# Kernel optimization log

Hardware: AMD Instinct MI355X
Metric: run time of the kernel (lower is better)

Reference implementation:

```python
import jax, jax.numpy as jnp
import numpy as np

B, K, D, H, R, MAXP, IMG = 8, 1024, 256, 8, 4, 1024, 224


def _ln(x, g, b, eps=1e-5):
    m = x.mean(-1, keepdims=True)
    v = ((x - m) ** 2).mean(-1, keepdims=True)
    return (x - m) / jnp.sqrt(v + eps) * g + b


def _rope2d(x, coords, cache, image_size):
    b, k, d = x.shape
    half, quarter = d // 2, d // 4
    maxp = cache.shape[0]
    cn = jnp.clip(coords.astype(jnp.float32) / image_size * (maxp - 1), 0, maxp - 1)
    y_idx = cn[..., 0].astype(jnp.int32)
    x_idx = cn[..., 1].astype(jnp.int32)
    yr = cache[y_idx]  # [B,K,quarter,2]
    xr = cache[x_idx]
    xp = x[..., :half].reshape(b, k, quarter, 2)
    yp = x[..., half:].reshape(b, k, quarter, 2)

    def rot(p, r):
        c, s = r[..., 0], r[..., 1]
        p0, p1 = p[..., 0], p[..., 1]
        return jnp.stack([p0 * c - p1 * s, p0 * s + p1 * c], -1).reshape(b, k, half)

    return jnp.concatenate([rot(xp, xr), rot(yp, yr)], -1)


def _mha_zero(xn, Wqkv, bqkv, Wo, bo, key_allowed, num_heads):
    # torch MultiheadAttention with an all-zero token appended to key/value
    # BEFORE projection -> extra key = b_k, extra value = b_v per head.
    b, l, d = xn.shape
    hd = d // num_heads
    Wq, Wk, Wv = jnp.split(Wqkv, 3, axis=0)
    bq, bk, bv = jnp.split(bqkv, 3)
    q = (xn @ Wq.T + bq).reshape(b, l, num_heads, hd)
    k = jnp.concatenate([xn @ Wk.T + bk, jnp.broadcast_to(bk, (b, 1, d))], 1)
    v = jnp.concatenate([xn @ Wv.T + bv, jnp.broadcast_to(bv, (b, 1, d))], 1)
    k = k.reshape(b, l + 1, num_heads, hd)
    v = v.reshape(b, l + 1, num_heads, hd)
    scores = jnp.einsum('bqhd,bkhd->bhqk', q, k) / jnp.sqrt(jnp.float32(hd))
    mask = jnp.concatenate([key_allowed, jnp.ones((b, 1), bool)], 1)  # zero slot always visible
    scores = jnp.where(mask[:, None, None, :], scores, -jnp.inf)
    attn = jax.nn.softmax(scores, axis=-1)
    out = jnp.einsum('bhqk,bkhd->bqhd', attn, v).reshape(b, l, d)
    return out @ Wo.T + bo


def setup_inputs() -> dict:
    key = jax.random.key(0)
    ks = jax.random.split(key, 20)
    x = jax.random.normal(ks[0], (B, K, D), dtype=jnp.float32)
    coords = jax.random.randint(ks[1], (B, K, 2), 0, IMG, dtype=jnp.int32)
    ctx_id_labels = jax.random.randint(ks[2], (B, K), 0, 2, dtype=jnp.int32)
    half = D // 2
    theta = 1.0 / (10000.0 ** (jnp.arange(0, half, 2, dtype=jnp.float32) / half))
    pos = jnp.arange(MAXP, dtype=jnp.float32)
    freqs = pos[:, None] * theta[None, :]
    rope_cache = jnp.stack([jnp.cos(freqs), jnp.sin(freqs)], -1)  # [MAXP, D/4, 2]
    s = 0.02
    return {
        'x': x, 'coords': coords, 'ctx_id_labels': ctx_id_labels,
        'target_embed': s * jax.random.normal(ks[3], (1, 1, D)),
        'context_embed': s * jax.random.normal(ks[4], (1, 1, D)),
        'register_tokens': s * jax.random.normal(ks[5], (1, R, D)),
        'rope_cache': rope_cache,
        'norm_g': jnp.ones((D,)), 'norm_b': jnp.zeros((D,)),
        'ctx_Wqkv': s * jax.random.normal(ks[6], (3 * D, D)),
        'ctx_bqkv': jnp.zeros((3 * D,)),
        'ctx_Wo': s * jax.random.normal(ks[7], (D, D)),
        'ctx_bo': jnp.zeros((D,)),
        'tgt_Wqkv': s * jax.random.normal(ks[8], (3 * D, D)),
        'tgt_bqkv': jnp.zeros((3 * D,)),
        'tgt_Wo': s * jax.random.normal(ks[9], (D, D)),
        'tgt_bo': jnp.zeros((D,)),
        'mlpn_g': jnp.ones((D,)), 'mlpn_b': jnp.zeros((D,)),
        'mlp_W1': s * jax.random.normal(ks[10], (4 * D, D)),
        'mlp_b1': jnp.zeros((4 * D,)),
        'mlp_W2': s * jax.random.normal(ks[11], (D, 4 * D)),
        'mlp_b2': jnp.zeros((D,)),
    }


def reference(x, coords, ctx_id_labels, target_embed, context_embed, register_tokens,
              rope_cache, norm_g, norm_b, ctx_Wqkv, ctx_bqkv, ctx_Wo, ctx_bo,
              tgt_Wqkv, tgt_bqkv, tgt_Wo, tgt_bo, mlpn_g, mlpn_b,
              mlp_W1, mlp_b1, mlp_W2, mlp_b2):
    b, k, d = x.shape
    is_ctx = ctx_id_labels > 0
    x = x + jnp.where(is_ctx[..., None], context_embed, target_embed)
    x = _rope2d(x, coords, rope_cache, IMG)
    registers = register_tokens + context_embed  # [1,R,D]
    x = jnp.concatenate([jnp.broadcast_to(registers, (b, R, d)), x], 1)
    is_ctx_f = jnp.concatenate([jnp.ones((b, R), bool), is_ctx], 1)
    xn = _ln(x, norm_g, norm_b)
    # ctx queries self-attend to context(+zero); tgt queries cross-attend to context(+zero)
    out_ctx = _mha_zero(xn, ctx_Wqkv, ctx_bqkv, ctx_Wo, ctx_bo, is_ctx_f, H)
    out_tgt = _mha_zero(xn, tgt_Wqkv, tgt_bqkv, tgt_Wo, tgt_bo, is_ctx_f, H)
    attn_out = jnp.where(is_ctx_f[..., None], out_ctx, out_tgt)
    attn_out = attn_out[:, R:]
    x = x[:, R:]
    x = x + attn_out
    h = _ln(x, mlpn_g, mlpn_b)
    h = jax.nn.gelu(h @ mlp_W1.T + mlp_b1, approximate=False) @ mlp_W2.T + mlp_b2
    return x + h
```

## Files before the change

### kernel.cpp

```cpp
#include <hip/hip_runtime.h>
#include <stdint.h>
#include <stddef.h>

typedef unsigned short u16;
typedef __bf16 bf16t;
typedef bf16t bf16x8 __attribute__((ext_vector_type(8)));
typedef u16 u16x8 __attribute__((ext_vector_type(8)));
typedef u16 u16x4 __attribute__((ext_vector_type(4)));
typedef float f32x4 __attribute__((ext_vector_type(4)));

__device__ __forceinline__ float bf2f(u16 u) {
  unsigned int x = ((unsigned int)u) << 16;
  return __builtin_bit_cast(float, x);
}
__device__ __forceinline__ u16 f2bf(float f) {
  unsigned int x = __builtin_bit_cast(unsigned int, f);
  x += 0x7fffu + ((x >> 16) & 1u);
  return (u16)(x >> 16);
}
__device__ __forceinline__ u16x8 ld8(const u16* p) { return *(const u16x8*)p; }

__device__ __forceinline__ f32x4 mfma_bf16(u16x8 a, u16x8 b, f32x4 c) {
  return __builtin_amdgcn_mfma_f32_16x16x32_bf16(
      __builtin_bit_cast(bf16x8, a), __builtin_bit_cast(bf16x8, b), c, 0, 0, 0);
}
__device__ __forceinline__ void g2lds16(const u16* g, u16* l) {
  __builtin_amdgcn_global_load_lds(
      (const __attribute__((address_space(1))) unsigned int*)g,
      (__attribute__((address_space(3))) unsigned int*)l, 16, 0, 0);
}
__device__ __forceinline__ void stc(u16* p, float v) { *p = f2bf(v); }
__device__ __forceinline__ void stc(float* p, float v) { *p = v; }

__device__ __forceinline__ float fast_erf(float x) {
  const float ax = fabsf(x);
  const float t = 1.0f / (1.0f + 0.3275911f * ax);
  const float y = 1.0f - (((((1.061405429f * t - 1.453152027f) * t) + 1.421413741f) * t
                  - 0.284496736f) * t + 0.254829592f) * t * __expf(-ax * ax);
  return copysignf(y, x);
}


__global__ __launch_bounds__(256) void cvt_kernel(
    const float* __restrict__ cW, const float* __restrict__ tW,
    const float* __restrict__ cWo_, const float* __restrict__ tWo_,
    const float* __restrict__ W1_, const float* __restrict__ W2_,
    const float* __restrict__ cb, const float* __restrict__ tb,
    u16* __restrict__ wA, u16* __restrict__ wB, u16* __restrict__ woc,
    u16* __restrict__ wot, u16* __restrict__ w1b, u16* __restrict__ w2b,
    float* __restrict__ bA, float* __restrict__ bB)
{
  const int blk = blockIdx.x;
  if (blk >= 1024) {
    const int e = threadIdx.x * 4;
    if (blk == 1024) {
      #pragma unroll
      for (int j = 0; j < 4; ++j) {
        const int k = e + j;
        bA[k] = (k < 768) ? cb[k] : tb[k - 512];
      }
    } else {
      #pragma unroll
      for (int j = 0; j < 4; ++j) {
        const int k = e + j;
        if (k < 256) bA[1024 + k] = tb[512 + k];
        else if (k < 512) bB[k - 256] = tb[k - 256];
      }
    }
    return;
  }
  const float* s; u16* d;
  if (blk < 192)      { const size_t e = (size_t)blk * 1024; s = cW + e; d = wA + e; }
  else if (blk < 384) { const int lb = blk - 192; const size_t e = (size_t)lb * 1024;
                        s = tW + e; d = (lb < 64) ? (wB + e) : (wA + e + 131072); }
  else if (blk < 448) { const size_t e = (size_t)(blk - 384) * 1024; s = cWo_ + e; d = woc + e; }
  else if (blk < 512) { const size_t e = (size_t)(blk - 448) * 1024; s = tWo_ + e; d = wot + e; }
  else if (blk < 768) { const size_t e = (size_t)(blk - 512) * 1024; s = W1_ + e; d = w1b + e; }
  else                { const size_t e = (size_t)(blk - 768) * 1024; s = W2_ + e; d = w2b + e; }
  const int o = threadIdx.x * 4;
  const f32x4 v = *(const f32x4*)(s + o);
  u16x4 ov;
  #pragma unroll
  for (int j = 0; j < 4; ++j) ov[j] = f2bf(v[j]);
  *(u16x4*)(d + o) = ov;
}

__global__ __launch_bounds__(1024) void compact_kernel(
    const int* __restrict__ labels, int* __restrict__ qcnt_c,
    int* __restrict__ qcnt_t, int* __restrict__ slotm,
    u16* __restrict__ xnc, u16* __restrict__ xnt)
{
  const int b = blockIdx.x, tid = threadIdx.x;
  const int wave = tid >> 6, lane = tid & 63;
  const bool ic = labels[b * 1024 + tid] > 0;
  const unsigned long long mask = __ballot(ic);
  const int lower = __popcll(mask & ((1ull << lane) - 1ull));
  const int wc = __popcll(mask);
  __shared__ int wcnt[16], woff[17];
  if (lane == 0) wcnt[wave] = wc;
  __syncthreads();
  if (tid == 0) {
    int acc = 0;
    #pragma unroll
    for (int i = 0; i < 16; ++i) { woff[i] = acc; acc += wcnt[i]; }
    woff[16] = acc;
  }
  __syncthreads();
  const int nc = woff[16], nt = 1024 - nc;
  const int rank = ic ? (woff[wave] + lower) : (tid - woff[wave] - lower);
  slotm[b * 1024 + tid] = rank;
  if (tid == 0) { qcnt_c[b] = nc; qcnt_t[b] = nt; }
  const int nc4 = nc + 4;
  const int needA = (nc4 + 127) & ~127;
  const int needB = (nt + 127) & ~127;
  const u16x8 z8 = {0, 0, 0, 0, 0, 0, 0, 0};
  for (int idx = tid; idx < (needA - nc4) * 32; idx += 1024)
    *(u16x8*)&xnc[((size_t)b * 1152 + nc4 + (idx >> 5)) * 256 + (idx & 31) * 8] = z8;
  for (int idx = tid; idx < (needB - nt) * 32; idx += 1024)
    *(u16x8*)&xnt[((size_t)b * 1024 + nt + (idx >> 5)) * 256 + (idx & 31) * 8] = z8;
}

__global__ __launch_bounds__(256) void prep_kernel(
    const float* __restrict__ x, const int* __restrict__ coords,
    const int* __restrict__ labels, const float* __restrict__ tgt_e,
    const float* __restrict__ ctx_e, const float* __restrict__ regs,
    const float* __restrict__ rope, const float* __restrict__ g,
    const float* __restrict__ bt, const int* __restrict__ slotm,
    float* __restrict__ x0, u16* __restrict__ xnc, u16* __restrict__ xnt)
{
  const int wv = threadIdx.x >> 6, lane = threadIdx.x & 63;
  const int t = blockIdx.x * 4 + wv;
  const int d = lane * 4;
  const int b = t / 1028, l = t - b * 1028;
  f32x4 v;
  u16* dst;
  if (l < 4) {
    const f32x4 rg = *(const f32x4*)&regs[l * 256 + d];
    const f32x4 ce = *(const f32x4*)&ctx_e[d];
    #pragma unroll
    for (int j = 0; j < 4; ++j) v[j] = rg[j] + ce[j];
    dst = &xnc[((size_t)b * 1152 + l) * 256];
  } else {
    const int p = l - 4;
    const bool ic = labels[b * 1024 + p] > 0;
    const float* emb = ic ? ctx_e : tgt_e;
    const int cy = coords[(b * 1024 + p) * 2 + 0];
    const int cx = coords[(b * 1024 + p) * 2 + 1];
    const float fy = fminf(fmaxf(((float)cy / 224.0f) * 1023.0f, 0.0f), 1023.0f);
    const float fx = fminf(fmaxf(((float)cx / 224.0f) * 1023.0f, 0.0f), 1023.0f);
    const int yi = (int)fy, xi = (int)fx;
    const bool second = d >= 128;
    const int ci = second ? yi : xi;
    const int pairi = (d & 127) >> 1;
    const f32x4 rr = *(const f32x4*)&rope[ci * 128 + pairi * 2];
    const int i0 = (second ? 128 : 0) + pairi * 2;
    const size_t base = (size_t)(b * 1024 + p) * 256;
    const f32x4 xv = *(const f32x4*)&x[base + i0];
    const f32x4 ev = *(const f32x4*)&emb[i0];
    const float p0 = xv[0] + ev[0], p1 = xv[1] + ev[1];
    const float p2 = xv[2] + ev[2], p3 = xv[3] + ev[3];
    v[0] = p0 * rr[0] - p1 * rr[1];
    v[1] = p0 * rr[1] + p1 * rr[0];
    v[2] = p2 * rr[2] - p3 * rr[3];
    v[3] = p2 * rr[3] + p3 * rr[2];
    const int rank = slotm[b * 1024 + p];
    dst = ic ? &xnc[((size_t)b * 1152 + 4 + rank) * 256]
             : &xnt[((size_t)b * 1024 + rank) * 256];
  }
  *(f32x4*)&x0[(size_t)t * 256 + d] = v;
  float s1 = v[0] + v[1] + v[2] + v[3];
  #pragma unroll
  for (int off = 1; off < 64; off <<= 1) s1 += __shfl_xor(s1, off);
  const float mean = s1 * (1.0f / 256.0f);
  f32x4 dv;
  float s2 = 0.f;
  #pragma unroll
  for (int j = 0; j < 4; ++j) { dv[j] = v[j] - mean; s2 += dv[j] * dv[j]; }
  #pragma unroll
  for (int off = 1; off < 64; off <<= 1) s2 += __shfl_xor(s2, off);
  const float rstd = rsqrtf(s2 * (1.0f / 256.0f) + 1e-5f);
  const f32x4 gv = *(const f32x4*)&g[d];
  const f32x4 bv = *(const f32x4*)&bt[d];
  u16x4 o;
  #pragma unroll
  for (int j = 0; j < 4; ++j) o[j] = f2bf(dv[j] * rstd * gv[j] + bv[j]);
  *(u16x4*)&dst[d] = o;
}

template <int EPI, typename CT>
__global__ __launch_bounds__(256) void gemm_bt(
    const u16* __restrict__ A, int lda, const u16* __restrict__ W, int K,
    const float* __restrict__ bias, CT* __restrict__ C, int ldc, int M,
    const float* __restrict__ resid, const int* __restrict__ bcnt)
{
  const int mbase = blockIdx.y * 128, nbase = blockIdx.x * 128;
  if (bcnt) {
    const int need = (bcnt[mbase >> 10] + 127) & ~127;
    if ((mbase & 1023) >= need) return;
  }
  __shared__ u16 As[128 * 32];
  __shared__ u16 Bs[128 * 32];
  const int tid = threadIdx.x, lane = tid & 63, w = tid >> 6;
  const int quad = lane >> 4, r = lane & 15;
  const int wm = w >> 1, wn = w & 1;
  const int rA = lane >> 2, cA = (lane & 3) * 8;

  f32x4 acc[4][4];
  #pragma unroll
  for (int i = 0; i < 4; ++i)
    #pragma unroll
    for (int j = 0; j < 4; ++j) acc[i][j] = (f32x4){0.f, 0.f, 0.f, 0.f};

  const int nkt = K >> 5;
  for (int kt = 0; kt < nkt; ++kt) {
    const int k0 = kt * 32;
    #pragma unroll
    for (int j = 0; j < 2; ++j) {
      const int rr = w * 32 + j * 16;
      g2lds16(&A[(size_t)(mbase + rr + rA) * lda + k0 + cA], &As[rr * 32]);
      g2lds16(&W[(size_t)(nbase + rr + rA) * K + k0 + cA], &Bs[rr * 32]);
    }
    __syncthreads();
    u16x8 av[4], bv[4];
    #pragma unroll
    for (int mi = 0; mi < 4; ++mi) av[mi] = ld8(&As[(wm * 64 + mi * 16 + r) * 32 + quad * 8]);
    #pragma unroll
    for (int ni = 0; ni < 4; ++ni) bv[ni] = ld8(&Bs[(wn * 64 + ni * 16 + r) * 32 + quad * 8]);
    #pragma unroll
    for (int mi = 0; mi < 4; ++mi)
      #pragma unroll
      for (int ni = 0; ni < 4; ++ni)
        acc[mi][ni] = mfma_bf16(av[mi], bv[ni], acc[mi][ni]);
    __syncthreads();
  }

  #pragma unroll
  for (int mi = 0; mi < 4; ++mi) {
    #pragma unroll
    for (int ni = 0; ni < 4; ++ni) {
      const int col = nbase + wn * 64 + ni * 16 + r;
      const float bs = bias[col];
      const int row0 = mbase + wm * 64 + mi * 16 + quad * 4;
      #pragma unroll
      for (int i = 0; i < 4; ++i) {
        const int rr2 = row0 + i;
        if (rr2 < M) {
          float v = acc[mi][ni][i] + bs;
          if (EPI == 1) v = 0.5f * v * (1.0f + fast_erf(v * 0.70710678118654752f));
          if (EPI == 2) v += resid[(size_t)rr2 * ldc + col];
          stc(&C[(size_t)rr2 * ldc + col], v);
        }
      }
    }
  }
}

__global__ __launch_bounds__(256) void gemm_qkvA(
    const u16* __restrict__ A, const u16* __restrict__ W,
    const float* __restrict__ bias, u16* __restrict__ qc,
    u16* __restrict__ kbuf, u16* __restrict__ vbufT,
    const int* __restrict__ qcnt_c)
{
  const int bidy = blockIdx.y;
  const int b = bidy / 9, mt = bidy - b * 9;
  const int need = (qcnt_c[b] + 4 + 127) & ~127;
  if (mt * 128 >= need) return;
  const int mbase = b * 1152 + mt * 128;
  const int nbase = blockIdx.x * 128;

  __shared__ u16 As[128 * 32];
  __shared__ u16 Bs[128 * 32];
  const int tid = threadIdx.x, lane = tid & 63, w = tid >> 6;
  const int quad = lane >> 4, r = lane & 15;
  const int wm = w >> 1, wn = w & 1;
  const int rA = lane >> 2, cA = (lane & 3) * 8;

  f32x4 acc[4][4];
  #pragma unroll
  for (int i = 0; i < 4; ++i)
    #pragma unroll
    for (int j = 0; j < 4; ++j) acc[i][j] = (f32x4){0.f, 0.f, 0.f, 0.f};

  for (int kt = 0; kt < 8; ++kt) {
    const int k0 = kt * 32;
    #pragma unroll
    for (int j = 0; j < 2; ++j) {
      const int rr = w * 32 + j * 16;
      g2lds16(&A[(size_t)(mbase + rr + rA) * 256 + k0 + cA], &As[rr * 32]);
      g2lds16(&W[(size_t)(nbase + rr + rA) * 256 + k0 + cA], &Bs[rr * 32]);
    }
    __syncthreads();
    u16x8 av[4], bv[4];
    #pragma unroll
    for (int mi = 0; mi < 4; ++mi) av[mi] = ld8(&As[(wm * 64 + mi * 16 + r) * 32 + quad * 8]);
    #pragma unroll
    for (int ni = 0; ni < 4; ++ni) bv[ni] = ld8(&Bs[(wn * 64 + ni * 16 + r) * 32 + quad * 8]);
    #pragma unroll
    for (int mi = 0; mi < 4; ++mi)
      #pragma unroll
      for (int ni = 0; ni < 4; ++ni)
        acc[mi][ni] = mfma_bf16(av[mi], bv[ni], acc[mi][ni]);
    __syncthreads();
  }

  #pragma unroll
  for (int mi = 0; mi < 4; ++mi) {
    #pragma unroll
    for (int ni = 0; ni < 4; ++ni) {
      const int col = nbase + wn * 64 + ni * 16 + r;
      const float bs = bias[col];
      const int row0 = mbase + wm * 64 + mi * 16 + quad * 4;
      const int slot0 = row0 - b * 1152;
      if (col < 256) {
        #pragma unroll
        for (int i = 0; i < 4; ++i)
          qc[(size_t)(row0 + i) * 256 + col] = f2bf(acc[mi][ni][i] + bs);
      } else {
        const int u = col - 256;
        const int z = u >> 9, kv = (u >> 8) & 1, h = (u >> 5) & 7, d = u & 31;
        const size_t zbh = (size_t)(z * 8 + b) * 8 + h;
        if (kv == 0) {
          u16* kp = kbuf + zbh * 36864 + (size_t)slot0 * 32 + d;
          #pragma unroll
          for (int i = 0; i < 4; ++i) kp[i * 32] = f2bf(acc[mi][ni][i] + bs);
        } else {
          u16x4 o;
          #pragma unroll
          for (int i = 0; i < 4; ++i) o[i] = f2bf(acc[mi][ni][i] + bs);
          *(u16x4*)(vbufT + (zbh * 32 + d) * 1152 + slot0) = o;
        }
      }
    }
  }
}

__global__ __launch_bounds__(256) void gemm_wo(
    const u16* __restrict__ Ac, const u16* __restrict__ At,
    const u16* __restrict__ Wc, const u16* __restrict__ Wt,
    const float* __restrict__ bc, const float* __restrict__ btg,
    u16* __restrict__ Cc, u16* __restrict__ Ct,
    const int* __restrict__ cnt_c, const int* __restrict__ cnt_t)
{
  const int z = blockIdx.z;
  const int mbase = blockIdx.y * 128, nbase = blockIdx.x * 128;
  const int* bcnt = z ? cnt_t : cnt_c;
  const int need = (bcnt[mbase >> 10] + 127) & ~127;
  if ((mbase & 1023) >= need) return;
  const u16* A = z ? At : Ac;
  const u16* W = z ? Wt : Wc;
  const float* bias = z ? btg : bc;
  u16* C = z ? Ct : Cc;

  __shared__ u16 As[128 * 32];
  __shared__ u16 Bs[128 * 32];
  const int tid = threadIdx.x, lane = tid & 63, w = tid >> 6;
  const int quad = lane >> 4, r = lane & 15;
  const int wm = w >> 1, wn = w & 1;
  const int rA = lane >> 2, cA = (lane & 3) * 8;

  f32x4 acc[4][4];
  #pragma unroll
  for (int i = 0; i < 4; ++i)
    #pragma unroll
    for (int j = 0; j < 4; ++j) acc[i][j] = (f32x4){0.f, 0.f, 0.f, 0.f};

  for (int kt = 0; kt < 8; ++kt) {
    const int k0 = kt * 32;
    #pragma unroll
    for (int j = 0; j < 2; ++j) {
      const int rr = w * 32 + j * 16;
      g2lds16(&A[(size_t)(mbase + rr + rA) * 256 + k0 + cA], &As[rr * 32]);
      g2lds16(&W[(size_t)(nbase + rr + rA) * 256 + k0 + cA], &Bs[rr * 32]);
    }
    __syncthreads();
    u16x8 av[4], bv[4];
    #pragma unroll
    for (int mi = 0; mi < 4; ++mi) av[mi] = ld8(&As[(wm * 64 + mi * 16 + r) * 32 + quad * 8]);
    #pragma unroll
    for (int ni = 0; ni < 4; ++ni) bv[ni] = ld8(&Bs[(wn * 64 + ni * 16 + r) * 32 + quad * 8]);
    #pragma unroll
    for (int mi = 0; mi < 4; ++mi)
      #pragma unroll
      for (int ni = 0; ni < 4; ++ni)
        acc[mi][ni] = mfma_bf16(av[mi], bv[ni], acc[mi][ni]);
    __syncthreads();
  }

  #pragma unroll
  for (int mi = 0; mi < 4; ++mi) {
    #pragma unroll
    for (int ni = 0; ni < 4; ++ni) {
      const int col = nbase + wn * 64 + ni * 16 + r;
      const float bs = bias[col];
      const int row0 = mbase + wm * 64 + mi * 16 + quad * 4;
      #pragma unroll
      for (int i = 0; i < 4; ++i)
        C[(size_t)(row0 + i) * 256 + col] = f2bf(acc[mi][ni][i] + bs);
    }
  }
}

__global__ __launch_bounds__(256) void attn4_kernel(
    const u16* __restrict__ qc, const u16* __restrict__ qt,
    const u16* __restrict__ kbuf, const u16* __restrict__ vbufT,
    const float* __restrict__ cbq, const float* __restrict__ tbq,
    const int* __restrict__ qcnt_c, const int* __restrict__ qcnt_t,
    u16* __restrict__ o_c, u16* __restrict__ o_t)
{
  const int qbx = blockIdx.x, h = blockIdx.y, b = blockIdx.z;
  const int nc = qcnt_c[b], nt = qcnt_t[b];
  const int cblk = (nc + 63) >> 6, tblk = (nt + 63) >> 6;
  int z, qsb, qn;
  if (qbx < cblk)            { z = 0; qsb = qbx << 6; qn = nc; }
  else if (qbx - cblk < tblk){ z = 1; qsb = (qbx - cblk) << 6; qn = nt; }
  else return;
  const int nc4 = nc + 4;
  const int ntile = (nc4 + 63) >> 6;
  const float* bq = z ? tbq : cbq;
  const u16* Q = z ? qt : qc;
  u16* obuf = z ? o_t : o_c;
  const int qrow0 = z ? (b * 1024 + qsb) : (b * 1152 + 4 + qsb);

  const int tid = threadIdx.x, lane = tid & 63, w = tid >> 6;
  const int quad = lane >> 4, r = lane & 15;
  const float scale = 0.17677669529663687f;

  __shared__ u16 Ks[64 * 32];
  __shared__ u16 Vt[32 * 66];
  __shared__ u16 Ps[4][16 * 72];

  const u16x8 qf = ld8(&Q[(size_t)(qrow0 + w * 16 + r) * 256 + h * 32 + quad * 8]);

  float s0 = 0.f;
  #pragma unroll
  for (int j = 0; j < 8; ++j) s0 += bf2f(qf[j]) * bq[256 + h * 32 + quad * 8 + j];
  s0 *= scale;
  s0 += __shfl_xor(s0, 16);
  s0 += __shfl_xor(s0, 32);
  float m_ = s0, l_ = 1.0f;
  f32x4 accA, accB;
  #pragma unroll
  for (int i = 0; i < 4; ++i) {
    accA[i] = bq[512 + h * 32 + quad * 4 + i];
    accB[i] = bq[512 + h * 32 + 16 + quad * 4 + i];
  }

  const size_t zbh = (size_t)(z * 8 + b) * 8 + h;
  const u16* kz = kbuf + zbh * 36864;
  const u16* vz = vbufT + zbh * 36864;
  const int dloc = (w << 3) + (lane >> 3), part = lane & 7;

  for (int t = 0; t < ntile; ++t) {
    __syncthreads();
    g2lds16(&kz[t * 2048 + w * 512 + lane * 8], &Ks[w * 512]);
    const u16x8 vv = ld8(&vz[(size_t)dloc * 1152 + t * 64 + part * 8]);
    *(u16x8*)&Vt[dloc * 66 + part * 8] = vv;
    __syncthreads();

    f32x4 sT[4];
    #pragma unroll
    for (int tt = 0; tt < 4; ++tt) {
      const u16x8 kf = ld8(&Ks[(tt * 16 + r) * 32 + quad * 8]);
      sT[tt] = mfma_bf16(kf, qf, (f32x4){0.f, 0.f, 0.f, 0.f});
    }
    const int kb0 = t * 64 + quad * 4;
    float rm = -3.0e38f;
    float sc[4][4];
    #pragma unroll
    for (int tt = 0; tt < 4; ++tt)
      #pragma unroll
      for (int i = 0; i < 4; ++i) {
        const float kbias = (kb0 + tt * 16 + i < nc4) ? 0.0f : -1e30f;
        sc[tt][i] = sT[tt][i] * scale + kbias;
        rm = fmaxf(rm, sc[tt][i]);
      }
    rm = fmaxf(rm, __shfl_xor(rm, 16));
    rm = fmaxf(rm, __shfl_xor(rm, 32));
    const float mn = fmaxf(m_, rm);
    const float al = __expf(m_ - mn);
    m_ = mn;
    float rs = 0.f;
    u16* ps = &Ps[w][r * 72];
    #pragma unroll
    for (int tt = 0; tt < 4; ++tt) {
      u16x4 pk;
      #pragma unroll
      for (int i = 0; i < 4; ++i) {
        const float pv = __expf(sc[tt][i] - mn);
        rs += pv;
        pk[i] = f2bf(pv);
      }
      *(u16x4*)&ps[tt * 16 + quad * 4] = pk;
    }
    rs += __shfl_xor(rs, 16);
    rs += __shfl_xor(rs, 32);
    l_ = l_ * al + rs;
    #pragma unroll
    for (int i = 0; i < 4; ++i) { accA[i] *= al; accB[i] *= al; }
    #pragma unroll
    for (int kk = 0; kk < 2; ++kk) {
      const u16x8 pf = ld8(&Ps[w][r * 72 + kk * 32 + quad * 8]);
      const u16x8 vf0 = ld8(&Vt[r * 66 + kk * 32 + quad * 8]);
      const u16x8 vf1 = ld8(&Vt[(16 + r) * 66 + kk * 32 + quad * 8]);
      accA = mfma_bf16(vf0, pf, accA);
      accB = mfma_bf16(vf1, pf, accB);
    }
  }

  const int qlocal = qsb + w * 16 + r;
  if (qlocal < qn) {
    const float inv = 1.0f / l_;
    u16x4 oa, ob;
    #pragma unroll
    for (int i = 0; i < 4; ++i) { oa[i] = f2bf(accA[i] * inv); ob[i] = f2bf(accB[i] * inv); }
    const size_t orow = (size_t)b * 1024 + qlocal;
    *(u16x4*)&obuf[orow * 256 + h * 32 + quad * 4] = oa;
    *(u16x4*)&obuf[orow * 256 + h * 32 + 16 + quad * 4] = ob;
  }
}

__global__ __launch_bounds__(256) void select_ln_kernel(
    const float* __restrict__ x0, const u16* __restrict__ po_c,
    const u16* __restrict__ po_t, const int* __restrict__ labels,
    const int* __restrict__ slotm, const float* __restrict__ g,
    const float* __restrict__ bt, float* __restrict__ x1,
    u16* __restrict__ hln)
{
  const int wv = threadIdx.x >> 6, lane = threadIdx.x & 63;
  const int t = blockIdx.x * 4 + wv;
  const int d = lane * 4;
  const int b = t >> 10;
  const size_t row = (size_t)b * 1028 + 4 + (t & 1023);
  const bool ic = labels[t] > 0;
  const u16* po = ic ? po_c : po_t;
  const int slot = slotm[t];
  const f32x4 xv = *(const f32x4*)&x0[row * 256 + d];
  const u16x4 pv = *(const u16x4*)&po[((size_t)b * 1024 + slot) * 256 + d];
  f32x4 v;
  #pragma unroll
  for (int j = 0; j < 4; ++j) v[j] = xv[j] + bf2f(pv[j]);
  *(f32x4*)&x1[(size_t)t * 256 + d] = v;
  float s1 = v[0] + v[1] + v[2] + v[3];
  #pragma unroll
  for (int off = 1; off < 64; off <<= 1) s1 += __shfl_xor(s1, off);
  const float mean = s1 * (1.0f / 256.0f);
  f32x4 dv;
  float s2 = 0.f;
  #pragma unroll
  for (int j = 0; j < 4; ++j) { dv[j] = v[j] - mean; s2 += dv[j] * dv[j]; }
  #pragma unroll
  for (int off = 1; off < 64; off <<= 1) s2 += __shfl_xor(s2, off);
  const float rstd = rsqrtf(s2 * (1.0f / 256.0f) + 1e-5f);
  const f32x4 gv = *(const f32x4*)&g[d];
  const f32x4 bv = *(const f32x4*)&bt[d];
  u16x4 o;
  #pragma unroll
  for (int j = 0; j < 4; ++j) o[j] = f2bf(dv[j] * rstd * gv[j] + bv[j]);
  *(u16x4*)&hln[(size_t)t * 256 + d] = o;
}

extern "C" void kernel_launch(void* const* d_in, const int* in_sizes, int n_in,
                              void* d_out, int out_size, void* d_ws, size_t ws_size,
                              hipStream_t stream) {
  const float* x      = (const float*)d_in[0];
  const int*   coords = (const int*)d_in[1];
  const int*   labels = (const int*)d_in[2];
  const float* tgt_e  = (const float*)d_in[3];
  const float* ctx_e  = (const float*)d_in[4];
  const float* regs   = (const float*)d_in[5];
  const float* rope   = (const float*)d_in[6];
  const float* ng     = (const float*)d_in[7];
  const float* nb     = (const float*)d_in[8];
  const float* cWqkv  = (const float*)d_in[9];
  const float* cbqkv  = (const float*)d_in[10];
  const float* cWo    = (const float*)d_in[11];
  const float* cbo    = (const float*)d_in[12];
  const float* tWqkv  = (const float*)d_in[13];
  const float* tbqkv  = (const float*)d_in[14];
  const float* tWo    = (const float*)d_in[15];
  const float* tbo    = (const float*)d_in[16];
  const float* mg     = (const float*)d_in[17];
  const float* mbeta  = (const float*)d_in[18];
  const float* W1     = (const float*)d_in[19];
  const float* b1     = (const float*)d_in[20];
  const float* W2     = (const float*)d_in[21];
  const float* b2     = (const float*)d_in[22];

  char* ws = (char*)d_ws;
  float* x0     = (float*)(ws + 0);
  u16*   qc     = (u16*)  (ws + 8421376);
  u16*   xnc    = (u16*)  (ws + 13139968);
  u16*   xnt    = (u16*)  (ws + 17858560);
  u16*   qt     = (u16*)  (ws + 22052864);
  u16*   kbuf   = (u16*)  (ws + 26247168);
  u16*   vbufT  = (u16*)  (ws + 35684352);
  u16*   o_c    = (u16*)  (ws + 45121536);
  u16*   o_t    = (u16*)  (ws + 49315840);
  u16*   wA     = (u16*)  (ws + 57704448);
  u16*   wB     = (u16*)  (ws + 58359808);
  u16*   woc    = (u16*)  (ws + 58490880);
  u16*   wot    = (u16*)  (ws + 58621952);
  u16*   w1b    = (u16*)  (ws + 58753024);
  u16*   w2b    = (u16*)  (ws + 59277312);
  float* bA     = (float*)(ws + 59801600);
  float* bB     = (float*)(ws + 59806720);
  int*   slotm  = (int*)  (ws + 59807744);
  int*   qcnt_c = (int*)  (ws + 59840512);
  int*   qcnt_t = (int*)  (ws + 59840544);
  u16*   po_c   = (u16*)  (ws + 8421376);
  u16*   po_t   = (u16*)  (ws + 13139968);
  u16*   hmid   = (u16*)  (ws + 22052864);
  u16*   hln    = (u16*)  (ws + 45121536);
  float* x1     = (float*)(ws + 49315840);

  cvt_kernel<<<dim3(1026), 256, 0, stream>>>(cWqkv, tWqkv, cWo, tWo, W1, W2,
                                             cbqkv, tbqkv,
                                             wA, wB, woc, wot, w1b, w2b, bA, bB);
  compact_kernel<<<dim3(8), 1024, 0, stream>>>(labels, qcnt_c, qcnt_t, slotm, xnc, xnt);
  prep_kernel<<<dim3(2056), 256, 0, stream>>>(x, coords, labels, tgt_e, ctx_e,
                                              regs, rope, ng, nb, slotm, x0, xnc, xnt);
  gemm_qkvA<<<dim3(10, 72), 256, 0, stream>>>(xnc, wA, bA, qc, kbuf, vbufT, qcnt_c);
  gemm_bt<0, u16><<<dim3(2, 64), 256, 0, stream>>>(xnt, 256, wB, 256, bB, qt, 256, 8192, nullptr, qcnt_t);
  attn4_kernel<<<dim3(17, 8, 8), 256, 0, stream>>>(qc, qt, kbuf, vbufT, cbqkv, tbqkv,
                                                   qcnt_c, qcnt_t, o_c, o_t);
  gemm_wo<<<dim3(2, 64, 2), 256, 0, stream>>>(o_c, o_t, woc, wot, cbo, tbo, po_c, po_t, qcnt_c, qcnt_t);
  select_ln_kernel<<<dim3(2048), 256, 0, stream>>>(x0, po_c, po_t, labels, slotm, mg, mbeta, x1, hln);
  gemm_bt<1, u16><<<dim3(8, 64), 256, 0, stream>>>(hln, 256, w1b, 256, b1, hmid, 1024, 8192, nullptr, nullptr);
  gemm_bt<2, float><<<dim3(2, 64), 256, 0, stream>>>(hmid, 1024, w2b, 1024, b2, (float*)d_out, 256, 8192, x1, nullptr);
}
```

Baseline: 250.2 us.

## Fuse compaction into cvt, merge QKV GEMMs, shrink tiles, double-buffer attention K/V

Moves the per-batch label compaction into extra blocks of the weight-conversion kernel, which removes one launch. Merges the context and target QKV projections into one launch. Halves the M tile of the Wo and MLP2 GEMMs (MI template parameter) so those small-N GEMMs launch more blocks. Double-buffers the K/V tiles in the attention loop so the next tile's loads overlap the current compute. Together these aim to cut launch count and raise occupancy, at the cost of more shared memory in attention and a serial four-pass scan in the compaction blocks.

```diff
diff --git a/kernel.cpp b/kernel.cpp
--- a/kernel.cpp
+++ b/kernel.cpp
@@ -48,11 +48,46 @@
     const float* __restrict__ cb, const float* __restrict__ tb,
     u16* __restrict__ wA, u16* __restrict__ wB, u16* __restrict__ woc,
     u16* __restrict__ wot, u16* __restrict__ w1b, u16* __restrict__ w2b,
-    float* __restrict__ bA, float* __restrict__ bB)
+    float* __restrict__ bA, float* __restrict__ bB,
+    const int* __restrict__ labels, int* __restrict__ slotm,
+    int* __restrict__ qcnt_c, int* __restrict__ qcnt_t,
+    u16* __restrict__ xnc, u16* __restrict__ xnt)
 {
   const int blk = blockIdx.x;
+  const int tid = threadIdx.x;
+  if (blk >= 1026) {
+    const int b = blk - 1026;
+    const int wave = tid >> 6, lane = tid & 63;
+    __shared__ int wcnt[4];
+    int base_c = 0, base_t = 0;
+    for (int p = 0; p < 4; ++p) {
+      const int idx = p * 256 + tid;
+      const bool ic = labels[b * 1024 + idx] > 0;
+      const unsigned long long mk = __ballot(ic);
+      const int lower = __popcll(mk & ((1ull << lane) - 1ull));
+      if (lane == 0) wcnt[wave] = __popcll(mk);
+      __syncthreads();
+      int off = 0, tot = 0;
+      #pragma unroll
+      for (int i = 0; i < 4; ++i) { if (i < wave) off += wcnt[i]; tot += wcnt[i]; }
+      slotm[b * 1024 + idx] = ic ? (base_c + off + lower)
+                                 : (base_t + tid - off - lower);
+      base_c += tot; base_t += 256 - tot;
+      __syncthreads();
+    }
+    if (tid == 0) { qcnt_c[b] = base_c; qcnt_t[b] = base_t; }
+    const int nc4 = base_c + 4;
+    const int needA = (nc4 + 127) & ~127;
+    const int needB = (base_t + 127) & ~127;
+    const u16x8 z8 = {0, 0, 0, 0, 0, 0, 0, 0};
+    for (int idx = tid; idx < (needA - nc4) * 32; idx += 256)
+      *(u16x8*)&xnc[((size_t)b * 1152 + nc4 + (idx >> 5)) * 256 + (idx & 31) * 8] = z8;
+    for (int idx = tid; idx < (needB - base_t) * 32; idx += 256)
+      *(u16x8*)&xnt[((size_t)b * 1024 + base_t + (idx >> 5)) * 256 + (idx & 31) * 8] = z8;
+    return;
+  }
   if (blk >= 1024) {
-    const int e = threadIdx.x * 4;
+    const int e = tid * 4;
     if (blk == 1024) {
       #pragma unroll
       for (int j = 0; j < 4; ++j) {
@@ -77,47 +112,12 @@
   else if (blk < 512) { const size_t e = (size_t)(blk - 448) * 1024; s = tWo_ + e; d = wot + e; }
   else if (blk < 768) { const size_t e = (size_t)(blk - 512) * 1024; s = W1_ + e; d = w1b + e; }
   else                { const size_t e = (size_t)(blk - 768) * 1024; s = W2_ + e; d = w2b + e; }
-  const int o = threadIdx.x * 4;
+  const int o = tid * 4;
   const f32x4 v = *(const f32x4*)(s + o);
   u16x4 ov;
   #pragma unroll
   for (int j = 0; j < 4; ++j) ov[j] = f2bf(v[j]);
   *(u16x4*)(d + o) = ov;
-}
-
-__global__ __launch_bounds__(1024) void compact_kernel(
-    const int* __restrict__ labels, int* __restrict__ qcnt_c,
-    int* __restrict__ qcnt_t, int* __restrict__ slotm,
-    u16* __restrict__ xnc, u16* __restrict__ xnt)
-{
-  const int b = blockIdx.x, tid = threadIdx.x;
-  const int wave = tid >> 6, lane = tid & 63;
-  const bool ic = labels[b * 1024 + tid] > 0;
-  const unsigned long long mask = __ballot(ic);
-  const int lower = __popcll(mask & ((1ull << lane) - 1ull));
-  const int wc = __popcll(mask);
-  __shared__ int wcnt[16], woff[17];
-  if (lane == 0) wcnt[wave] = wc;
-  __syncthreads();
-  if (tid == 0) {
-    int acc = 0;
-    #pragma unroll
-    for (int i = 0; i < 16; ++i) { woff[i] = acc; acc += wcnt[i]; }
-    woff[16] = acc;
-  }
-  __syncthreads();
-  const int nc = woff[16], nt = 1024 - nc;
-  const int rank = ic ? (woff[wave] + lower) : (tid - woff[wave] - lower);
-  slotm[b * 1024 + tid] = rank;
-  if (tid == 0) { qcnt_c[b] = nc; qcnt_t[b] = nt; }
-  const int nc4 = nc + 4;
-  const int needA = (nc4 + 127) & ~127;
-  const int needB = (nt + 127) & ~127;
-  const u16x8 z8 = {0, 0, 0, 0, 0, 0, 0, 0};
-  for (int idx = tid; idx < (needA - nc4) * 32; idx += 1024)
-    *(u16x8*)&xnc[((size_t)b * 1152 + nc4 + (idx >> 5)) * 256 + (idx & 31) * 8] = z8;
-  for (int idx = tid; idx < (needB - nt) * 32; idx += 1024)
-    *(u16x8*)&xnt[((size_t)b * 1024 + nt + (idx >> 5)) * 256 + (idx & 31) * 8] = z8;
 }
 
 __global__ __launch_bounds__(256) void prep_kernel(
@@ -187,27 +187,24 @@
   *(u16x4*)&dst[d] = o;
 }
 
-template <int EPI, typename CT>
+template <int MI, int EPI, typename CT>
 __global__ __launch_bounds__(256) void gemm_bt(
     const u16* __restrict__ A, int lda, const u16* __restrict__ W, int K,
     const float* __restrict__ bias, CT* __restrict__ C, int ldc, int M,
-    const float* __restrict__ resid, const int* __restrict__ bcnt)
+    const float* __restrict__ resid)
 {
-  const int mbase = blockIdx.y * 128, nbase = blockIdx.x * 128;
-  if (bcnt) {
-    const int need = (bcnt[mbase >> 10] + 127) & ~127;
-    if ((mbase & 1023) >= need) return;
-  }
-  __shared__ u16 As[128 * 32];
+  constexpr int TM = MI * 32;
+  const int mbase = blockIdx.y * TM, nbase = blockIdx.x * 128;
+  __shared__ u16 As[TM * 32];
   __shared__ u16 Bs[128 * 32];
   const int tid = threadIdx.x, lane = tid & 63, w = tid >> 6;
   const int quad = lane >> 4, r = lane & 15;
   const int wm = w >> 1, wn = w & 1;
   const int rA = lane >> 2, cA = (lane & 3) * 8;
 
-  f32x4 acc[4][4];
-  #pragma unroll
-  for (int i = 0; i < 4; ++i)
+  f32x4 acc[MI][4];
+  #pragma unroll
+  for (int i = 0; i < MI; ++i)
     #pragma unroll
     for (int j = 0; j < 4; ++j) acc[i][j] = (f32x4){0.f, 0.f, 0.f, 0.f};
 
@@ -215,19 +212,23 @@
   for (int kt = 0; kt < nkt; ++kt) {
     const int k0 = kt * 32;
     #pragma unroll
+    for (int j = 0; j < MI / 2; ++j) {
+      const int rr = w * (MI * 8) + j * 16;
+      g2lds16(&A[(size_t)(mbase + rr + rA) * lda + k0 + cA], &As[rr * 32]);
+    }
+    #pragma unroll
     for (int j = 0; j < 2; ++j) {
       const int rr = w * 32 + j * 16;
-      g2lds16(&A[(size_t)(mbase + rr + rA) * lda + k0 + cA], &As[rr * 32]);
       g2lds16(&W[(size_t)(nbase + rr + rA) * K + k0 + cA], &Bs[rr * 32]);
     }
     __syncthreads();
-    u16x8 av[4], bv[4];
-    #pragma unroll
-    for (int mi = 0; mi < 4; ++mi) av[mi] = ld8(&As[(wm * 64 + mi * 16 + r) * 32 + quad * 8]);
+    u16x8 av[MI], bv[4];
+    #pragma unroll
+    for (int mi = 0; mi < MI; ++mi) av[mi] = ld8(&As[(wm * (MI * 16) + mi * 16 + r) * 32 + quad * 8]);
     #pragma unroll
     for (int ni = 0; ni < 4; ++ni) bv[ni] = ld8(&Bs[(wn * 64 + ni * 16 + r) * 32 + quad * 8]);
     #pragma unroll
-    for (int mi = 0; mi < 4; ++mi)
+    for (int mi = 0; mi < MI; ++mi)
       #pragma unroll
       for (int ni = 0; ni < 4; ++ni)
         acc[mi][ni] = mfma_bf16(av[mi], bv[ni], acc[mi][ni]);
@@ -235,12 +236,12 @@
   }
 
   #pragma unroll
-  for (int mi = 0; mi < 4; ++mi) {
+  for (int mi = 0; mi < MI; ++mi) {
     #pragma unroll
     for (int ni = 0; ni < 4; ++ni) {
       const int col = nbase + wn * 64 + ni * 16 + r;
       const float bs = bias[col];
-      const int row0 = mbase + wm * 64 + mi * 16 + quad * 4;
+      const int row0 = mbase + wm * (MI * 16) + mi * 16 + quad * 4;
       #pragma unroll
       for (int i = 0; i < 4; ++i) {
         const int rr2 = row0 + i;
@@ -255,18 +256,36 @@
   }
 }
 
-__global__ __launch_bounds__(256) void gemm_qkvA(
-    const u16* __restrict__ A, const u16* __restrict__ W,
-    const float* __restrict__ bias, u16* __restrict__ qc,
+__global__ __launch_bounds__(256) void gemm_qkv(
+    const u16* __restrict__ xnc, const u16* __restrict__ xnt,
+    const u16* __restrict__ wA, const u16* __restrict__ wB,
+    const float* __restrict__ bA, const float* __restrict__ bB,
+    u16* __restrict__ qc, u16* __restrict__ qt,
     u16* __restrict__ kbuf, u16* __restrict__ vbufT,
-    const int* __restrict__ qcnt_c)
+    const int* __restrict__ qcnt_c, const int* __restrict__ qcnt_t)
 {
-  const int bidy = blockIdx.y;
-  const int b = bidy / 9, mt = bidy - b * 9;
-  const int need = (qcnt_c[b] + 4 + 127) & ~127;
-  if (mt * 128 >= need) return;
-  const int mbase = b * 1152 + mt * 128;
+  const int y = blockIdx.y;
   const int nbase = blockIdx.x * 128;
+  const u16 *Ap, *Wp; const float* bp;
+  int mbase, b;
+  bool tgt;
+  if (y < 72) {
+    tgt = false;
+    b = y / 9; const int mt = y - b * 9;
+    const int need = (qcnt_c[b] + 4 + 127) & ~127;
+    if (mt * 128 >= need) return;
+    mbase = b * 1152 + mt * 128;
+    Ap = xnc; Wp = wA; bp = bA;
+  } else {
+    if (nbase >= 256) return;
+    tgt = true;
+    const int yy = y - 72;
+    b = yy >> 3; const int mt = yy & 7;
+    const int need = (qcnt_t[b] + 127) & ~127;
+    if (mt * 128 >= need) return;
+    mbase = b * 1024 + mt * 128;
+    Ap = xnt; Wp = wB; bp = bB;
+  }
 
   __shared__ u16 As[128 * 32];
   __shared__ u16 Bs[128 * 32];
@@ -286,8 +305,8 @@
     #pragma unroll
     for (int j = 0; j < 2; ++j) {
       const int rr = w * 32 + j * 16;
-      g2lds16(&A[(size_t)(mbase + rr + rA) * 256 + k0 + cA], &As[rr * 32]);
-      g2lds16(&W[(size_t)(nbase + rr + rA) * 256 + k0 + cA], &Bs[rr * 32]);
+      g2lds16(&Ap[(size_t)(mbase + rr + rA) * 256 + k0 + cA], &As[rr * 32]);
+      g2lds16(&Wp[(size_t)(nbase + rr + rA) * 256 + k0 + cA], &Bs[rr * 32]);
     }
     __syncthreads();
     u16x8 av[4], bv[4];
@@ -308,14 +327,18 @@
     #pragma unroll
     for (int ni = 0; ni < 4; ++ni) {
       const int col = nbase + wn * 64 + ni * 16 + r;
-      const float bs = bias[col];
+      const float bs = bp[col];
       const int row0 = mbase + wm * 64 + mi * 16 + quad * 4;
-      const int slot0 = row0 - b * 1152;
-      if (col < 256) {
+      if (tgt) {
+        #pragma unroll
+        for (int i = 0; i < 4; ++i)
+          qt[(size_t)(row0 + i) * 256 + col] = f2bf(acc[mi][ni][i] + bs);
+      } else if (col < 256) {
         #pragma unroll
         for (int i = 0; i < 4; ++i)
           qc[(size_t)(row0 + i) * 256 + col] = f2bf(acc[mi][ni][i] + bs);
       } else {
+        const int slot0 = row0 - b * 1152;
         const int u = col - 256;
         const int z = u >> 9, kv = (u >> 8) & 1, h = (u >> 5) & 7, d = u & 31;
         const size_t zbh = (size_t)(z * 8 + b) * 8 + h;
@@ -342,44 +365,45 @@
     const int* __restrict__ cnt_c, const int* __restrict__ cnt_t)
 {
   const int z = blockIdx.z;
-  const int mbase = blockIdx.y * 128, nbase = blockIdx.x * 128;
+  const int y = blockIdx.y, b = y >> 4, mt = y & 15;
   const int* bcnt = z ? cnt_t : cnt_c;
-  const int need = (bcnt[mbase >> 10] + 127) & ~127;
-  if ((mbase & 1023) >= need) return;
+  const int need = (bcnt[b] + 63) & ~63;
+  if (mt * 64 >= need) return;
+  const int mbase = b * 1024 + mt * 64, nbase = blockIdx.x * 128;
   const u16* A = z ? At : Ac;
   const u16* W = z ? Wt : Wc;
   const float* bias = z ? btg : bc;
   u16* C = z ? Ct : Cc;
 
-  __shared__ u16 As[128 * 32];
+  __shared__ u16 As[64 * 32];
   __shared__ u16 Bs[128 * 32];
   const int tid = threadIdx.x, lane = tid & 63, w = tid >> 6;
   const int quad = lane >> 4, r = lane & 15;
   const int wm = w >> 1, wn = w & 1;
   const int rA = lane >> 2, cA = (lane & 3) * 8;
 
-  f32x4 acc[4][4];
-  #pragma unroll
-  for (int i = 0; i < 4; ++i)
+  f32x4 acc[2][4];
+  #pragma unroll
+  for (int i = 0; i < 2; ++i)
     #pragma unroll
     for (int j = 0; j < 4; ++j) acc[i][j] = (f32x4){0.f, 0.f, 0.f, 0.f};
 
   for (int kt = 0; kt < 8; ++kt) {
     const int k0 = kt * 32;
+    g2lds16(&A[(size_t)(mbase + w * 16 + rA) * 256 + k0 + cA], &As[w * 512]);
     #pragma unroll
     for (int j = 0; j < 2; ++j) {
       const int rr = w * 32 + j * 16;
-      g2lds16(&A[(size_t)(mbase + rr + rA) * 256 + k0 + cA], &As[rr * 32]);
       g2lds16(&W[(size_t)(nbase + rr + rA) * 256 + k0 + cA], &Bs[rr * 32]);
     }
     __syncthreads();
-    u16x8 av[4], bv[4];
-    #pragma unroll
-    for (int mi = 0; mi < 4; ++mi) av[mi] = ld8(&As[(wm * 64 + mi * 16 + r) * 32 + quad * 8]);
+    u16x8 av[2], bv[4];
+    #pragma unroll
+    for (int mi = 0; mi < 2; ++mi) av[mi] = ld8(&As[(wm * 32 + mi * 16 + r) * 32 + quad * 8]);
     #pragma unroll
     for (int ni = 0; ni < 4; ++ni) bv[ni] = ld8(&Bs[(wn * 64 + ni * 16 + r) * 32 + quad * 8]);
     #pragma unroll
-    for (int mi = 0; mi < 4; ++mi)
+    for (int mi = 0; mi < 2; ++mi)
       #pragma unroll
       for (int ni = 0; ni < 4; ++ni)
         acc[mi][ni] = mfma_bf16(av[mi], bv[ni], acc[mi][ni]);
@@ -387,12 +411,12 @@
   }
 
   #pragma unroll
-  for (int mi = 0; mi < 4; ++mi) {
+  for (int mi = 0; mi < 2; ++mi) {
     #pragma unroll
     for (int ni = 0; ni < 4; ++ni) {
       const int col = nbase + wn * 64 + ni * 16 + r;
       const float bs = bias[col];
-      const int row0 = mbase + wm * 64 + mi * 16 + quad * 4;
+      const int row0 = mbase + wm * 32 + mi * 16 + quad * 4;
       #pragma unroll
       for (int i = 0; i < 4; ++i)
         C[(size_t)(row0 + i) * 256 + col] = f2bf(acc[mi][ni][i] + bs);
@@ -425,8 +449,8 @@
   const int quad = lane >> 4, r = lane & 15;
   const float scale = 0.17677669529663687f;
 
-  __shared__ u16 Ks[64 * 32];
-  __shared__ u16 Vt[32 * 66];
+  __shared__ u16 Ks[2][2048];
+  __shared__ u16 Vt[2][32 * 66];
   __shared__ u16 Ps[4][16 * 72];
 
   const u16x8 qf = ld8(&Q[(size_t)(qrow0 + w * 16 + r) * 256 + h * 32 + quad * 8]);
@@ -450,17 +474,23 @@
   const u16* vz = vbufT + zbh * 36864;
   const int dloc = (w << 3) + (lane >> 3), part = lane & 7;
 
+  g2lds16(&kz[w * 512 + lane * 8], &Ks[0][w * 512]);
+  u16x8 vv = ld8(&vz[(size_t)dloc * 1152 + part * 8]);
+
   for (int t = 0; t < ntile; ++t) {
+    const int cur = t & 1, nxt = cur ^ 1;
+    #pragma unroll
+    for (int j = 0; j < 8; ++j) Vt[cur][dloc * 66 + part * 8 + j] = vv[j];
     __syncthreads();
-    g2lds16(&kz[t * 2048 + w * 512 + lane * 8], &Ks[w * 512]);
-    const u16x8 vv = ld8(&vz[(size_t)dloc * 1152 + t * 64 + part * 8]);
-    *(u16x8*)&Vt[dloc * 66 + part * 8] = vv;
-    __syncthreads();
+    if (t + 1 < ntile) {
+      g2lds16(&kz[(t + 1) * 2048 + w * 512 + lane * 8], &Ks[nxt][w * 512]);
+      vv = ld8(&vz[(size_t)dloc * 1152 + (t + 1) * 64 + part * 8]);
+    }
 
     f32x4 sT[4];
     #pragma unroll
     for (int tt = 0; tt < 4; ++tt) {
-      const u16x8 kf = ld8(&Ks[(tt * 16 + r) * 32 + quad * 8]);
+      const u16x8 kf = ld8(&Ks[cur][(tt * 16 + r) * 32 + quad * 8]);
       sT[tt] = mfma_bf16(kf, qf, (f32x4){0.f, 0.f, 0.f, 0.f});
     }
     const int kb0 = t * 64 + quad * 4;
@@ -500,8 +530,8 @@
     #pragma unroll
     for (int kk = 0; kk < 2; ++kk) {
       const u16x8 pf = ld8(&Ps[w][r * 72 + kk * 32 + quad * 8]);
-      const u16x8 vf0 = ld8(&Vt[r * 66 + kk * 32 + quad * 8]);
-      const u16x8 vf1 = ld8(&Vt[(16 + r) * 66 + kk * 32 + quad * 8]);
+      const u16x8 vf0 = ld8(&Vt[cur][r * 66 + kk * 32 + quad * 8]);
+      const u16x8 vf1 = ld8(&Vt[cur][(16 + r) * 66 + kk * 32 + quad * 8]);
       accA = mfma_bf16(vf0, pf, accA);
       accB = mfma_bf16(vf1, pf, accB);
     }
@@ -613,18 +643,19 @@
   u16*   hln    = (u16*)  (ws + 45121536);
   float* x1     = (float*)(ws + 49315840);
 
-  cvt_kernel<<<dim3(1026), 256, 0, stream>>>(cWqkv, tWqkv, cWo, tWo, W1, W2,
+  cvt_kernel<<<dim3(1034), 256, 0, stream>>>(cWqkv, tWqkv, cWo, tWo, W1, W2,
                                              cbqkv, tbqkv,
-                                             wA, wB, woc, wot, w1b, w2b, bA, bB);
-  compact_kernel<<<dim3(8), 1024, 0, stream>>>(labels, qcnt_c, qcnt_t, slotm, xnc, xnt);
+                                             wA, wB, woc, wot, w1b, w2b, bA, bB,
+                                             labels, slotm, qcnt_c, qcnt_t, xnc, xnt);
   prep_kernel<<<dim3(2056), 256, 0, stream>>>(x, coords, labels, tgt_e, ctx_e,
                                               regs, rope, ng, nb, slotm, x0, xnc, xnt);
-  gemm_qkvA<<<dim3(10, 72), 256, 0, stream>>>(xnc, wA, bA, qc, kbuf, vbufT, qcnt_c);
-  gemm_bt<0, u16><<<dim3(2, 64), 256, 0, stream>>>(xnt, 256, wB, 256, bB, qt, 256, 8192, nullptr, qcnt_t);
+  gemm_qkv<<<dim3(10, 136), 256, 0, stream>>>(xnc, xnt, wA, wB, bA, bB,
+                                              qc, qt, kbuf, vbufT, qcnt_c, qcnt_t);
   attn4_kernel<<<dim3(17, 8, 8), 256, 0, stream>>>(qc, qt, kbuf, vbufT, cbqkv, tbqkv,
                                                    qcnt_c, qcnt_t, o_c, o_t);
-  gemm_wo<<<dim3(2, 64, 2), 256, 0, stream>>>(o_c, o_t, woc, wot, cbo, tbo, po_c, po_t, qcnt_c, qcnt_t);
+  gemm_wo<<<dim3(2, 128, 2), 256, 0, stream>>>(o_c, o_t, woc, wot, cbo, tbo,
+                                               po_c, po_t, qcnt_c, qcnt_t);
   select_ln_kernel<<<dim3(2048), 256, 0, stream>>>(x0, po_c, po_t, labels, slotm, mg, mbeta, x1, hln);
-  gemm_bt<1, u16><<<dim3(8, 64), 256, 0, stream>>>(hln, 256, w1b, 256, b1, hmid, 1024, 8192, nullptr, nullptr);
-  gemm_bt<2, float><<<dim3(2, 64), 256, 0, stream>>>(hmid, 1024, w2b, 1024, b2, (float*)d_out, 256, 8192, x1, nullptr);
-}
+  gemm_bt<4, 1, u16><<<dim3(8, 64), 256, 0, stream>>>(hln, 256, w1b, 256, b1, hmid, 1024, 8192, nullptr);
+  gemm_bt<2, 2, float><<<dim3(2, 128), 256, 0, stream>>>(hmid, 1024, w2b, 1024, b2, (float*)d_out, 256, 8192, x1);
+}
```

Measured after the change: 222.9 us. 1.12x faster.
